# Kernel optimization log

Measured on AMD Instinct MI355X. Metric: run time of the kernel, lower is better.

Reference implementation:

```python
import jax, jax.numpy as jnp
import numpy as np

B = 64        # batch
N = 1024      # num_nodes
D_IN = 2      # input feature dim per node
U = 64        # num_units (hidden)
K = 2         # max_diffusion_step


def setup_inputs() -> dict:
    key = jax.random.key(0)
    ks = jax.random.split(key, 8)
    inputs = jax.random.normal(ks[0], (B, N * D_IN), dtype=jnp.float32)
    hx = jax.random.normal(ks[1], (B, N * U), dtype=jnp.float32)
    # random-walk style supports: nonnegative, row-normalized -> stable Chebyshev recursion
    a0 = jax.random.uniform(ks[2], (N, N), dtype=jnp.float32)
    a1 = jax.random.uniform(ks[3], (N, N), dtype=jnp.float32)
    support0 = a0 / jnp.sum(a0, axis=1, keepdims=True)
    support1 = a1 / jnp.sum(a1, axis=1, keepdims=True)
    num_matrices = 2 * K + 1            # len(supports)*K + 1 = 5
    in_sz = (D_IN + U) * num_matrices   # 330
    # xavier-normal init
    std_o = float(np.sqrt(2.0 / (in_sz + 2 * U)))
    std_u = float(np.sqrt(2.0 / (in_sz + U)))
    weights_output = jax.random.normal(ks[4], (in_sz, 2 * U), dtype=jnp.float32) * std_o
    weights_update = jax.random.normal(ks[5], (in_sz, U), dtype=jnp.float32) * std_u
    biases_output = jnp.ones((2 * U,), dtype=jnp.float32)
    biases_update = jnp.zeros((U,), dtype=jnp.float32)
    return {"inputs": inputs, "hx": hx, "support0": support0, "support1": support1,
            "weights_output": weights_output, "biases_output": biases_output,
            "weights_update": weights_update, "biases_update": biases_update}


def _gconv(x_cat, supports, W, b, out_size):
    # x_cat: [B, N, F]  -> Chebyshev diffusion series then dense projection
    Bsz, Nn, F = x_cat.shape
    x0 = x_cat.transpose(1, 2, 0).reshape(Nn, F * Bsz)  # [N, F*B]
    xs = [x0]
    for S in supports:
        x1 = S @ x0
        xs.append(x1)
        xk1, xk2 = x1, x0
        for _ in range(2, K + 1):
            x2 = 2.0 * (S @ xk1) - xk2
            xs.append(x2)
            xk1, xk2 = x2, xk1
    M = len(xs)                                         # num_matrices
    x = jnp.stack(xs, axis=0)                           # [M, N, F*B]
    x = x.reshape(M, Nn, F, Bsz).transpose(3, 1, 2, 0)  # [B, N, F, M]
    x = x.reshape(Bsz * Nn, F * M)
    y = x @ W + b                                       # [B*N, out_size]
    return y.reshape(Bsz, Nn * out_size)


def reference(inputs, hx, support0, support1, weights_output, biases_output,
              weights_update, biases_update):
    supports = (support0, support1)
    xi = inputs.reshape(B, N, D_IN)
    hs = hx.reshape(B, N, U)
    cat = jnp.concatenate([xi, hs], axis=2)             # [B, N, D_IN+U]
    value = jax.nn.sigmoid(_gconv(cat, supports, weights_output, biases_output, 2 * U))
    value = value.reshape(B, N, 2 * U)
    r = value[..., :U].reshape(B, N * U)
    u = value[..., U:].reshape(B, N * U)
    cat2 = jnp.concatenate([xi, (r * hx).reshape(B, N, U)], axis=2)
    c = jnp.tanh(_gconv(cat2, supports, weights_update, biases_update, U))
    return u * hx + (1.0 - u) * c
```

## Files before the change

### kernel.cpp

```cpp
#include <hip/hip_runtime.h>


typedef unsigned short u16;
typedef unsigned int u32;
typedef short s16x8 __attribute__((ext_vector_type(8)));
typedef float f32x4 __attribute__((ext_vector_type(4)));
typedef u16 u16x4 __attribute__((ext_vector_type(4)));

#define NN 1024
#define NB 64
#define NF 66
#define NCOLS 4224
#define KPAD 352
#define ASTRIDE 360

__device__ __forceinline__ u16 f2bf(float f) {
  u32 u = __builtin_bit_cast(u32, f);
  u = (u + 0x7fffu + ((u >> 16) & 1u)) >> 16;
  return (u16)u;
}
__device__ __forceinline__ float bf2f(u16 h) {
  u32 u = ((u32)h) << 16;
  return __builtin_bit_cast(float, u);
}

__device__ __forceinline__ void gload16(const void* g, void* l) {
  __builtin_amdgcn_global_load_lds(
      (const __attribute__((address_space(1))) u32*)g,
      (__attribute__((address_space(3))) u32*)l, 16, 0, 0);
}

#define CHEB_WAIT(N)                                      \
  do {                                                    \
    asm volatile("s_waitcnt vmcnt(" #N ")" ::: "memory"); \
    __builtin_amdgcn_s_barrier();                         \
    asm volatile("" ::: "memory");                        \
  } while (0)


__global__ __launch_bounds__(256) void pack_supports(
    const float* __restrict__ s0, const float* __restrict__ s1,
    u16* __restrict__ d0, u16* __restrict__ d1) {
  int i = (blockIdx.x * 256 + threadIdx.x) * 4;
  f32x4 a = *(const f32x4*)(s0 + i);
  f32x4 b = *(const f32x4*)(s1 + i);
  u16x4 oa, ob;
  oa.x = f2bf(a.x); oa.y = f2bf(a.y); oa.z = f2bf(a.z); oa.w = f2bf(a.w);
  ob.x = f2bf(b.x); ob.y = f2bf(b.y); ob.z = f2bf(b.z); ob.w = f2bf(b.w);
  *(u16x4*)(d0 + i) = oa;
  *(u16x4*)(d1 + i) = ob;
}

__global__ __launch_bounds__(64) void pack_wf(
    const float* __restrict__ Wo, const float* __restrict__ Wu,
    u16* __restrict__ WF1, u16* __restrict__ WF2) {
  const int c = blockIdx.x;
  int j = blockIdx.y;
  const float* W; u16* WF; int ldo, nj;
  if (j < 8) { W = Wo; WF = WF1; ldo = 128; nj = 8; }
  else       { j -= 8; W = Wu; WF = WF2; ldo = 64; nj = 4; }
  const int lane = threadIdx.x;
  const int o = j * 16 + (lane & 15);
  const int kpb = c * 32 + (lane >> 4) * 8;
  u16 vals[8];
#pragma unroll
  for (int e = 0; e < 8; e++) {
    const int kp = kpb + e;
    float v = 0.f;
    if (kp < 330) {
      const int m = kp / 66;
      const int f = kp - m * 66;
      const float* Wrow = W + (size_t)(f * 5) * ldo + o;
      if (m == 0)      v = Wrow[0] - Wrow[2 * ldo] - Wrow[4 * ldo];
      else if (m == 2) v = 2.f * Wrow[2 * ldo];
      else if (m == 4) v = 2.f * Wrow[4 * ldo];
      else             v = Wrow[(size_t)m * ldo];
    }
    vals[e] = f2bf(v);
  }
  u16* dst = WF + (((size_t)(c * nj + j) << 6) + lane) * 8;
#pragma unroll
  for (int e = 0; e < 8; e++) dst[e] = vals[e];
}

__global__ __launch_bounds__(256) void pack_x0(
    const float* __restrict__ inp, const float* __restrict__ hx,
    u16* __restrict__ x0t, u16* __restrict__ x0pt) {
  __shared__ float tile[64][65];
  int n0 = blockIdx.x * 64, b = blockIdx.y, t = threadIdx.x;
  if (t < 32) {
    const int f = t >> 4;
    const int n4 = (t & 15) * 4;
    const float* src = inp + b * 2048 + (n0 + n4) * 2 + f;
    u16x4 o;
    o.x = f2bf(src[0]); o.y = f2bf(src[2]); o.z = f2bf(src[4]); o.w = f2bf(src[6]);
    size_t off = (size_t)(f * 64 + b) * NN + n0 + n4;
    *(u16x4*)(x0t + off) = o;
    *(u16x4*)(x0pt + off) = o;
  }
  int u4 = (t & 15) * 4, r0 = t >> 4;
#pragma unroll
  for (int p = 0; p < 4; p++) {
    int row = p * 16 + r0;
    f32x4 v = *(const f32x4*)(hx + ((size_t)b << 16) + (size_t)(n0 + row) * 64 + u4);
    tile[row][u4] = v.x; tile[row][u4 + 1] = v.y;
    tile[row][u4 + 2] = v.z; tile[row][u4 + 3] = v.w;
  }
  __syncthreads();
  int n4 = (t & 15) * 4, uu0 = t >> 4;
#pragma unroll
  for (int p = 0; p < 4; p++) {
    int u = p * 16 + uu0;
    u16x4 o;
    o.x = f2bf(tile[n4][u]);     o.y = f2bf(tile[n4 + 1][u]);
    o.z = f2bf(tile[n4 + 2][u]); o.w = f2bf(tile[n4 + 3][u]);
    *(u16x4*)&x0t[(size_t)((2 + u) * 64 + b) * NN + n0 + n4] = o;
  }
}


__global__ __launch_bounds__(256, 3) void cheb_gemm(
    const u16* __restrict__ S0, const u16* __restrict__ S1,
    const u16* __restrict__ Xi0, const u16* __restrict__ Xi1,
    u16* __restrict__ Xo0, u16* __restrict__ Xo1) {
  __shared__ u16 As[3][128 * 32];
  __shared__ u16 Bs[3][128 * 32];
  const int t = threadIdx.x;
  const int lane = t & 63;
  const int w = t >> 6;

  const int lid = blockIdx.x;
  const int work = (lid & 7) * 66 + (lid >> 3);
  const int y = work & 7;
  const int tt = work >> 3;
  const int x = tt % 33;
  const int z = tt / 33;
  const int n0 = x * 128;
  const int m0 = y * 128;
  const u16* S = z ? S1 : S0;
  const u16* Xi = z ? Xi1 : Xi0;
  u16* Xo = z ? Xo1 : Xo0;

  const int swz = ((lane & 3) ^ ((lane >> 3) & 3)) * 8;
  const int rl = lane >> 2;
  const u16* pA0 = S + (size_t)(m0 + w * 32 + rl) * NN + swz;
  const u16* pA1 = pA0 + (size_t)16 * NN;
  const u16* pB0 = Xi + (size_t)(n0 + w * 32 + rl) * NN + swz;
  const u16* pB1 = pB0 + (size_t)16 * NN;
  const int db0 = (w * 32) * 32;
  const int db1 = (w * 32 + 16) * 32;

  const int wm = (w >> 1) * 64;
  const int wn = (w & 1) * 64;
  const int fr = lane & 15;
  const int q = lane >> 4;
  const int fo = (q ^ ((fr >> 1) & 3)) * 8;

  f32x4 acc[4][4];
#pragma unroll
  for (int i = 0; i < 4; i++)
#pragma unroll
    for (int j = 0; j < 4; j++) acc[i][j] = f32x4{0.f, 0.f, 0.f, 0.f};

  auto stage = [&](u16* dA, u16* dB) {
    gload16(pA0, dA + db0);
    gload16(pA1, dA + db1);
    gload16(pB0, dB + db0);
    gload16(pB1, dB + db1);
    pA0 += 32; pA1 += 32; pB0 += 32; pB1 += 32;
  };
  auto compute = [&](const u16* cA, const u16* cB) {
    s16x8 af[4], bfr[4];
#pragma unroll
    for (int i = 0; i < 4; i++)
      af[i] = *(const s16x8*)&cA[(wm + i * 16 + fr) * 32 + fo];
#pragma unroll
    for (int j = 0; j < 4; j++)
      bfr[j] = *(const s16x8*)&cB[(wn + j * 16 + fr) * 32 + fo];
#pragma unroll
    for (int i = 0; i < 4; i++)
#pragma unroll
      for (int j = 0; j < 4; j++)
        acc[i][j] = __builtin_amdgcn_mfma_f32_16x16x32_bf16(af[i], bfr[j], acc[i][j], 0, 0, 0);
  };

  u16* a0 = &As[0][0]; u16* a1 = &As[1][0]; u16* a2 = &As[2][0];
  u16* b0 = &Bs[0][0]; u16* b1 = &Bs[1][0]; u16* b2 = &Bs[2][0];

  stage(a0, b0);
  stage(a1, b1);
#pragma unroll 1
  for (int it = 0; it < 10; it++) {
    CHEB_WAIT(4); stage(a2, b2); compute(a0, b0);
    CHEB_WAIT(4); stage(a0, b0); compute(a1, b1);
    CHEB_WAIT(4); stage(a1, b1); compute(a2, b2);
  }
  CHEB_WAIT(4); compute(a0, b0);
  CHEB_WAIT(0); compute(a1, b1);

  const int nr0 = (lane >> 4) << 2;
#pragma unroll
  for (int i = 0; i < 4; i++) {
    const int node = m0 + wm + i * 16 + nr0;
#pragma unroll
    for (int j = 0; j < 4; j++) {
      const int colg = n0 + wn + j * 16 + fr;
      size_t off = (size_t)colg * NN + node;
      f32x4 c = acc[i][j];
      u16x4 o;
      o.x = f2bf(c.x); o.y = f2bf(c.y); o.z = f2bf(c.z); o.w = f2bf(c.w);
      *(u16x4*)&Xo[off] = o;
    }
  }
}


__device__ __forceinline__ void proj_stage(
    u16* A, const u16* __restrict__ X0, const u16* __restrict__ X1,
    const u16* __restrict__ X2, const u16* __restrict__ X3,
    const u16* __restrict__ X4, int b, int n0, int t) {
  u16x4 v[6][4];
#pragma unroll
  for (int i = 0; i < 6; i++) {
    const int idx = t + i * 256;
    if (idx < 1408) {
      const int kp0 = (idx >> 4) * 4;
      const int n4 = (idx & 15) * 4;
#pragma unroll
      for (int r = 0; r < 4; r++) {
        const int kp = kp0 + r;
        if (kp < 330) {
          const int m = kp / 66;
          const int f = kp - m * 66;
          const u16* Xm = m == 0 ? X0 : m == 1 ? X1 : m == 2 ? X2 : m == 3 ? X3 : X4;
          v[i][r] = *(const u16x4*)(Xm + (size_t)(f * 64 + b) * NN + n0 + n4);
        } else {
          v[i][r] = u16x4{0, 0, 0, 0};
        }
      }
    }
  }
#pragma unroll
  for (int i = 0; i < 6; i++) {
    const int idx = t + i * 256;
    if (idx < 1408) {
      const int kp0 = (idx >> 4) * 4;
      const int n4 = (idx & 15) * 4;
#pragma unroll
      for (int c = 0; c < 4; c++) {
        u16x4 o;
        o.x = v[i][0][c]; o.y = v[i][1][c]; o.z = v[i][2][c]; o.w = v[i][3][c];
        *(u16x4*)&A[(n4 + c) * ASTRIDE + kp0] = o;
      }
    }
  }
}

__global__ __launch_bounds__(256) void proj1(
    const u16* __restrict__ X0, const u16* __restrict__ X1, const u16* __restrict__ X2,
    const u16* __restrict__ X3, const u16* __restrict__ X4,
    const u16* __restrict__ WF, const float* __restrict__ bias,
    const float* __restrict__ hx, u16* __restrict__ X0p, float* __restrict__ uout) {
  __shared__ u16 A[64 * ASTRIDE];
  const int t = threadIdx.x;
  const int n0 = blockIdx.x * 64;
  const int b = blockIdx.y;
  proj_stage(A, X0, X1, X2, X3, X4, b, n0, t);
  __syncthreads();

  const int lane = t & 63;
  const int w = t >> 6;
  const int fr = lane & 15;
  const int q8 = (lane >> 4) * 8;
  const int nb = (w >> 1) * 32;
  const int jh = w & 1;
  const u16* arow = &A[(nb + fr) * ASTRIDE + q8];
  const u16* wfl = WF + (size_t)lane * 8;

  f32x4 acc[2][4];
#pragma unroll
  for (int ii = 0; ii < 2; ii++)
#pragma unroll
    for (int j = 0; j < 4; j++) acc[ii][j] = f32x4{0.f, 0.f, 0.f, 0.f};

  for (int c = 0; c < 11; c++) {
    s16x8 af[2];
#pragma unroll
    for (int ii = 0; ii < 2; ii++)
      af[ii] = *(const s16x8*)(arow + ii * 16 * ASTRIDE + c * 32);
#pragma unroll
    for (int j = 0; j < 4; j++) {
      const s16x8 bf = *(const s16x8*)(wfl + ((c * 8 + jh * 4 + j) << 9));
#pragma unroll
      for (int ii = 0; ii < 2; ii++)
        acc[ii][j] = __builtin_amdgcn_mfma_f32_16x16x32_bf16(af[ii], bf, acc[ii][j], 0, 0, 0);
    }
  }

  const int nl0 = (lane >> 4) * 4;
#pragma unroll
  for (int ii = 0; ii < 2; ii++) {
    const int n = n0 + nb + ii * 16 + nl0;
#pragma unroll
    for (int j = 0; j < 4; j++) {
      const int ol = j * 16 + fr;
      const float bs = bias[jh * 64 + ol];
      f32x4 v;
      v.x = 1.f / (1.f + __expf(-(acc[ii][j].x + bs)));
      v.y = 1.f / (1.f + __expf(-(acc[ii][j].y + bs)));
      v.z = 1.f / (1.f + __expf(-(acc[ii][j].z + bs)));
      v.w = 1.f / (1.f + __expf(-(acc[ii][j].w + bs)));
      if (jh == 0) {
        const float* hxp = hx + ((size_t)b << 16) + (size_t)n * 64 + ol;
        u16x4 s;
        s.x = f2bf(v.x * hxp[0 * 64]);
        s.y = f2bf(v.y * hxp[1 * 64]);
        s.z = f2bf(v.z * hxp[2 * 64]);
        s.w = f2bf(v.w * hxp[3 * 64]);
        *(u16x4*)&X0p[(size_t)((2 + ol) * 64 + b) * NN + n] = s;
      } else {
        float* up = uout + (((size_t)b << 10) + n) * 64 + ol;
        up[0 * 64] = v.x; up[1 * 64] = v.y; up[2 * 64] = v.z; up[3 * 64] = v.w;
      }
    }
  }
}

__global__ __launch_bounds__(256) void proj2(
    const u16* __restrict__ X0, const u16* __restrict__ X1, const u16* __restrict__ X2,
    const u16* __restrict__ X3, const u16* __restrict__ X4,
    const u16* __restrict__ WF, const float* __restrict__ bias,
    const float* __restrict__ hx, const float* uin, float* out) {
  __shared__ u16 A[64 * ASTRIDE];
  const int t = threadIdx.x;
  const int n0 = blockIdx.x * 64;
  const int b = blockIdx.y;
  proj_stage(A, X0, X1, X2, X3, X4, b, n0, t);
  __syncthreads();

  const int lane = t & 63;
  const int w = t >> 6;
  const int fr = lane & 15;
  const int q8 = (lane >> 4) * 8;
  const int nb = (w >> 1) * 32;
  const int jh = w & 1;
  const u16* arow = &A[(nb + fr) * ASTRIDE + q8];
  const u16* wfl = WF + (size_t)lane * 8;

  f32x4 acc[2][2];
#pragma unroll
  for (int ii = 0; ii < 2; ii++)
#pragma unroll
    for (int j = 0; j < 2; j++) acc[ii][j] = f32x4{0.f, 0.f, 0.f, 0.f};

  for (int c = 0; c < 11; c++) {
    s16x8 af[2];
#pragma unroll
    for (int ii = 0; ii < 2; ii++)
      af[ii] = *(const s16x8*)(arow + ii * 16 * ASTRIDE + c * 32);
#pragma unroll
    for (int j = 0; j < 2; j++) {
      const s16x8 bf = *(const s16x8*)(wfl + ((c * 4 + jh * 2 + j) << 9));
#pragma unroll
      for (int ii = 0; ii < 2; ii++)
        acc[ii][j] = __builtin_amdgcn_mfma_f32_16x16x32_bf16(af[ii], bf, acc[ii][j], 0, 0, 0);
    }
  }

  const int nl0 = (lane >> 4) * 4;
#pragma unroll
  for (int ii = 0; ii < 2; ii++) {
    const int n = n0 + nb + ii * 16 + nl0;
#pragma unroll
    for (int j = 0; j < 2; j++) {
      const int o = jh * 32 + j * 16 + fr;
      const float bs = bias[o];
      const size_t base = (((size_t)b << 10) + n) * 64 + o;
      float c0 = tanhf(acc[ii][j].x + bs);
      float c1 = tanhf(acc[ii][j].y + bs);
      float c2 = tanhf(acc[ii][j].z + bs);
      float c3 = tanhf(acc[ii][j].w + bs);
      float u0 = uin[base + 0 * 64], u1 = uin[base + 1 * 64];
      float u2 = uin[base + 2 * 64], u3 = uin[base + 3 * 64];
      float h0 = hx[base + 0 * 64], h1 = hx[base + 1 * 64];
      float h2 = hx[base + 2 * 64], h3 = hx[base + 3 * 64];
      out[base + 0 * 64] = u0 * h0 + (1.f - u0) * c0;
      out[base + 1 * 64] = u1 * h1 + (1.f - u1) * c1;
      out[base + 2 * 64] = u2 * h2 + (1.f - u2) * c2;
      out[base + 3 * 64] = u3 * h3 + (1.f - u3) * c3;
    }
  }
}


extern "C" void kernel_launch(void* const* d_in, const int* in_sizes, int n_in,
                              void* d_out, int out_size, void* d_ws, size_t ws_size,
                              hipStream_t stream) {
  (void)in_sizes; (void)n_in; (void)out_size; (void)ws_size;
  const float* inp = (const float*)d_in[0];
  const float* hx  = (const float*)d_in[1];
  const float* s0  = (const float*)d_in[2];
  const float* s1  = (const float*)d_in[3];
  const float* Wo  = (const float*)d_in[4];
  const float* bo  = (const float*)d_in[5];
  const float* Wu  = (const float*)d_in[6];
  const float* bu  = (const float*)d_in[7];
  float* out = (float*)d_out;

  char* p = (char*)d_ws;
  u16* Sb0 = (u16*)p; p += (size_t)NN * NN * 2;
  u16* Sb1 = (u16*)p; p += (size_t)NN * NN * 2;
  const size_t xbytes = (size_t)NCOLS * NN * 2;
  u16* X0T = (u16*)p; p += xbytes;
  u16* X1T = (u16*)p; p += xbytes;
  u16* X2T = (u16*)p; p += xbytes;
  u16* X3T = (u16*)p; p += xbytes;
  u16* X4T = (u16*)p; p += xbytes;
  u16* X0P = (u16*)p; p += xbytes;
  u16* WF1 = (u16*)p; p += (size_t)11 * 8 * 512 * 2;
  u16* WF2 = (u16*)p; p += (size_t)11 * 4 * 512 * 2;

  pack_supports<<<dim3(1024), dim3(256), 0, stream>>>(s0, s1, Sb0, Sb1);
  pack_wf<<<dim3(11, 12), dim3(64), 0, stream>>>(Wo, Wu, WF1, WF2);
  pack_x0<<<dim3(16, 64), dim3(256), 0, stream>>>(inp, hx, X0T, X0P);
  cheb_gemm<<<dim3(528), dim3(256), 0, stream>>>(Sb0, Sb1, X0T, X0T, X1T, X3T);
  cheb_gemm<<<dim3(528), dim3(256), 0, stream>>>(Sb0, Sb1, X1T, X3T, X2T, X4T);
  proj1<<<dim3(16, 64), dim3(256), 0, stream>>>(X0T, X1T, X2T, X3T, X4T, WF1, bo, hx, X0P, out);
  cheb_gemm<<<dim3(528), dim3(256), 0, stream>>>(Sb0, Sb1, X0P, X0P, X1T, X3T);
  cheb_gemm<<<dim3(528), dim3(256), 0, stream>>>(Sb0, Sb1, X1T, X3T, X2T, X4T);
  proj2<<<dim3(16, 64), dim3(256), 0, stream>>>(X0P, X1T, X2T, X3T, X4T, WF2, bu, hx, out, out);
}
```

Measured before the change: 266.9 us.

## Precompute squared supports so both diffusion steps run in one GEMM launch

Packing the supports now also writes a transposed bf16 copy, and a new GEMM forms S·S once per call. Each graph convolution then computes S·x0 and (S·S)·x0 in a single 1056-block launch instead of two dependent 528-block launches. This removes the serial dependency and one launch, and gives a larger grid with fewer tail effects. The cost is an extra 1024³ GEMM per support and some accuracy loss from rounding S² to bf16, which changes the rounding path of the second diffusion term.

```diff
diff --git a/kernel.cpp b/kernel.cpp
--- a/kernel.cpp
+++ b/kernel.cpp
@@ -40,15 +40,36 @@
 
 __global__ __launch_bounds__(256) void pack_supports(
     const float* __restrict__ s0, const float* __restrict__ s1,
-    u16* __restrict__ d0, u16* __restrict__ d1) {
-  int i = (blockIdx.x * 256 + threadIdx.x) * 4;
-  f32x4 a = *(const f32x4*)(s0 + i);
-  f32x4 b = *(const f32x4*)(s1 + i);
-  u16x4 oa, ob;
-  oa.x = f2bf(a.x); oa.y = f2bf(a.y); oa.z = f2bf(a.z); oa.w = f2bf(a.w);
-  ob.x = f2bf(b.x); ob.y = f2bf(b.y); ob.z = f2bf(b.z); ob.w = f2bf(b.w);
-  *(u16x4*)(d0 + i) = oa;
-  *(u16x4*)(d1 + i) = ob;
+    u16* __restrict__ d0, u16* __restrict__ d1,
+    u16* __restrict__ t0, u16* __restrict__ t1) {
+  __shared__ float tile[64][65];
+  const int z = blockIdx.y;
+  const float* S = z ? s1 : s0;
+  u16* D = z ? d1 : d0;
+  u16* T = z ? t1 : t0;
+  const int r0 = (blockIdx.x >> 4) * 64, c0 = (blockIdx.x & 15) * 64;
+  const int t = threadIdx.x;
+  int cc4 = (t & 15) * 4, rr = t >> 4;
+#pragma unroll
+  for (int p = 0; p < 4; p++) {
+    int r = p * 16 + rr;
+    f32x4 v = *(const f32x4*)(S + (size_t)(r0 + r) * NN + c0 + cc4);
+    tile[r][cc4] = v.x; tile[r][cc4 + 1] = v.y;
+    tile[r][cc4 + 2] = v.z; tile[r][cc4 + 3] = v.w;
+    u16x4 o;
+    o.x = f2bf(v.x); o.y = f2bf(v.y); o.z = f2bf(v.z); o.w = f2bf(v.w);
+    *(u16x4*)&D[(size_t)(r0 + r) * NN + c0 + cc4] = o;
+  }
+  __syncthreads();
+  int rr4 = (t & 15) * 4, cc = t >> 4;
+#pragma unroll
+  for (int p = 0; p < 4; p++) {
+    int c = p * 16 + cc;
+    u16x4 o;
+    o.x = f2bf(tile[rr4][c]);     o.y = f2bf(tile[rr4 + 1][c]);
+    o.z = f2bf(tile[rr4 + 2][c]); o.w = f2bf(tile[rr4 + 3][c]);
+    *(u16x4*)&T[(size_t)(c0 + c) * NN + r0 + rr4] = o;
+  }
 }
 
 __global__ __launch_bounds__(64) void pack_wf(
@@ -119,31 +140,15 @@
 }
 
 
-__global__ __launch_bounds__(256, 3) void cheb_gemm(
-    const u16* __restrict__ S0, const u16* __restrict__ S1,
-    const u16* __restrict__ Xi0, const u16* __restrict__ Xi1,
-    u16* __restrict__ Xo0, u16* __restrict__ Xo1) {
-  __shared__ u16 As[3][128 * 32];
-  __shared__ u16 Bs[3][128 * 32];
-  const int t = threadIdx.x;
+__device__ __forceinline__ void gemm128_core(
+    const u16* __restrict__ A, const u16* __restrict__ Xi, u16* __restrict__ Xo,
+    int m0, int n0, int t, u16* AsB, u16* BsB) {
   const int lane = t & 63;
   const int w = t >> 6;
 
-  const int lid = blockIdx.x;
-  const int work = (lid & 7) * 66 + (lid >> 3);
-  const int y = work & 7;
-  const int tt = work >> 3;
-  const int x = tt % 33;
-  const int z = tt / 33;
-  const int n0 = x * 128;
-  const int m0 = y * 128;
-  const u16* S = z ? S1 : S0;
-  const u16* Xi = z ? Xi1 : Xi0;
-  u16* Xo = z ? Xo1 : Xo0;
-
   const int swz = ((lane & 3) ^ ((lane >> 3) & 3)) * 8;
   const int rl = lane >> 2;
-  const u16* pA0 = S + (size_t)(m0 + w * 32 + rl) * NN + swz;
+  const u16* pA0 = A + (size_t)(m0 + w * 32 + rl) * NN + swz;
   const u16* pA1 = pA0 + (size_t)16 * NN;
   const u16* pB0 = Xi + (size_t)(n0 + w * 32 + rl) * NN + swz;
   const u16* pB1 = pB0 + (size_t)16 * NN;
@@ -184,8 +189,8 @@
         acc[i][j] = __builtin_amdgcn_mfma_f32_16x16x32_bf16(af[i], bfr[j], acc[i][j], 0, 0, 0);
   };
 
-  u16* a0 = &As[0][0]; u16* a1 = &As[1][0]; u16* a2 = &As[2][0];
-  u16* b0 = &Bs[0][0]; u16* b1 = &Bs[1][0]; u16* b2 = &Bs[2][0];
+  u16* a0 = AsB;  u16* a1 = AsB + 128 * 32;  u16* a2 = AsB + 2 * 128 * 32;
+  u16* b0 = BsB;  u16* b1 = BsB + 128 * 32;  u16* b2 = BsB + 2 * 128 * 32;
 
   stage(a0, b0);
   stage(a1, b1);
@@ -205,13 +210,50 @@
 #pragma unroll
     for (int j = 0; j < 4; j++) {
       const int colg = n0 + wn + j * 16 + fr;
-      size_t off = (size_t)colg * NN + node;
       f32x4 c = acc[i][j];
       u16x4 o;
       o.x = f2bf(c.x); o.y = f2bf(c.y); o.z = f2bf(c.z); o.w = f2bf(c.w);
-      *(u16x4*)&Xo[off] = o;
-    }
-  }
+      *(u16x4*)&Xo[(size_t)colg * NN + node] = o;
+    }
+  }
+}
+
+__global__ __launch_bounds__(256, 3) void sq_gemm(
+    const u16* __restrict__ S0, const u16* __restrict__ S1,
+    const u16* __restrict__ ST0, const u16* __restrict__ ST1,
+    u16* __restrict__ SS0, u16* __restrict__ SS1) {
+  __shared__ u16 As[3][128 * 32];
+  __shared__ u16 Bs[3][128 * 32];
+  const int lid = blockIdx.x;
+  const int work = (lid & 7) * 16 + (lid >> 3);
+  const int z = work >> 6;
+  const int rr = work & 63;
+  const int y = rr >> 3, x = rr & 7;
+  const u16* A = z ? ST1 : ST0;
+  const u16* Xi = z ? S1 : S0;
+  u16* Xo = z ? SS1 : SS0;
+  gemm128_core(A, Xi, Xo, y * 128, x * 128, threadIdx.x, &As[0][0], &Bs[0][0]);
+}
+
+__global__ __launch_bounds__(256, 3) void gconv_gemm(
+    const u16* __restrict__ S0, const u16* __restrict__ S1,
+    const u16* __restrict__ SS0, const u16* __restrict__ SS1,
+    const u16* __restrict__ Xi,
+    u16* __restrict__ X1, u16* __restrict__ X2,
+    u16* __restrict__ X3, u16* __restrict__ X4) {
+  __shared__ u16 As[3][128 * 32];
+  __shared__ u16 Bs[3][128 * 32];
+  const int lid = blockIdx.x;
+  const int h = lid >= 528;
+  const int l2 = h ? lid - 528 : lid;
+  const int work = (l2 & 7) * 66 + (l2 >> 3);
+  const int y = work & 7;
+  const int tt = work >> 3;
+  const int x = tt % 33;
+  const int z = tt / 33;
+  const u16* A = h ? (z ? SS1 : SS0) : (z ? S1 : S0);
+  u16* Xo = h ? (z ? X4 : X2) : (z ? X3 : X1);
+  gemm128_core(A, Xi, Xo, y * 128, x * 128, threadIdx.x, &As[0][0], &Bs[0][0]);
 }
 
 
@@ -410,6 +452,8 @@
   char* p = (char*)d_ws;
   u16* Sb0 = (u16*)p; p += (size_t)NN * NN * 2;
   u16* Sb1 = (u16*)p; p += (size_t)NN * NN * 2;
+  u16* SSb0 = (u16*)p; p += (size_t)NN * NN * 2;
+  u16* SSb1 = (u16*)p; p += (size_t)NN * NN * 2;
   const size_t xbytes = (size_t)NCOLS * NN * 2;
   u16* X0T = (u16*)p; p += xbytes;
   u16* X1T = (u16*)p; p += xbytes;
@@ -419,14 +463,17 @@
   u16* X0P = (u16*)p; p += xbytes;
   u16* WF1 = (u16*)p; p += (size_t)11 * 8 * 512 * 2;
   u16* WF2 = (u16*)p; p += (size_t)11 * 4 * 512 * 2;
-
-  pack_supports<<<dim3(1024), dim3(256), 0, stream>>>(s0, s1, Sb0, Sb1);
+  u16* ST0 = X1T;
+  u16* ST1 = X3T;
+
+  pack_supports<<<dim3(256, 2), dim3(256), 0, stream>>>(s0, s1, Sb0, Sb1, ST0, ST1);
+  sq_gemm<<<dim3(128), dim3(256), 0, stream>>>(Sb0, Sb1, ST0, ST1, SSb0, SSb1);
   pack_wf<<<dim3(11, 12), dim3(64), 0, stream>>>(Wo, Wu, WF1, WF2);
   pack_x0<<<dim3(16, 64), dim3(256), 0, stream>>>(inp, hx, X0T, X0P);
-  cheb_gemm<<<dim3(528), dim3(256), 0, stream>>>(Sb0, Sb1, X0T, X0T, X1T, X3T);
-  cheb_gemm<<<dim3(528), dim3(256), 0, stream>>>(Sb0, Sb1, X1T, X3T, X2T, X4T);
+  gconv_gemm<<<dim3(1056), dim3(256), 0, stream>>>(Sb0, Sb1, SSb0, SSb1, X0T,
+                                                   X1T, X2T, X3T, X4T);
   proj1<<<dim3(16, 64), dim3(256), 0, stream>>>(X0T, X1T, X2T, X3T, X4T, WF1, bo, hx, X0P, out);
-  cheb_gemm<<<dim3(528), dim3(256), 0, stream>>>(Sb0, Sb1, X0P, X0P, X1T, X3T);
-  cheb_gemm<<<dim3(528), dim3(256), 0, stream>>>(Sb0, Sb1, X1T, X3T, X2T, X4T);
+  gconv_gemm<<<dim3(1056), dim3(256), 0, stream>>>(Sb0, Sb1, SSb0, SSb1, X0P,
+                                                   X1T, X2T, X3T, X4T);
   proj2<<<dim3(16, 64), dim3(256), 0, stream>>>(X0P, X1T, X2T, X3T, X4T, WF2, bu, hx, out, out);
 }
```

Measured after the change: 269.8 us. No clear change (+1.1%).
